# Kernel optimization log

Hardware: AMD Instinct MI355X
Metric: run time of the kernel (lower is better)

The kernel has to match this reference:

```python
import jax, jax.numpy as jnp
import numpy as np

N_NEIGHBORS = 3


def square_distance(src, dst):
    # src: [B,N,3], dst: [B,M,3] -> [B,N,M]
    d = -2.0 * jnp.einsum('bnc,bmc->bnm', src, dst)
    d = d + jnp.sum(src * src, axis=-1)[:, :, None]
    d = d + jnp.sum(dst * dst, axis=-1)[:, None, :]
    return d


def setup_inputs() -> dict:
    key = jax.random.key(0)
    k1, k2, k3 = jax.random.split(key, 3)
    B, N_q, N_k, C = 4, 8192, 2048, 128
    xyz_q = jax.random.normal(k1, (B, N_q, 3), dtype=jnp.float32)
    xyz_k = jax.random.normal(k2, (B, N_k, 3), dtype=jnp.float32)
    v_k = jax.random.normal(k3, (B, N_k, C), dtype=jnp.float32)
    return {"xyz_q": xyz_q, "xyz_k": xyz_k, "v_k": v_k}


def reference(xyz_q, xyz_k, v_k):
    # pairwise squared distances [B,N_q,N_k]
    sqrdists = square_distance(xyz_q, xyz_k)
    # kNN: smallest nsample distances per query
    neg_dist, idx = jax.lax.top_k(-sqrdists, N_NEIGHBORS)  # [B,N_q,k]
    dist_nearest = jnp.take_along_axis(sqrdists, idx, axis=2)
    dist_nearest = jnp.maximum(dist_nearest, 1e-10)
    weights = 1.0 / dist_nearest
    weights = weights / jnp.sum(weights, axis=-1, keepdims=True)
    # gather neighbor features: [B,N_q,k,C]
    grouped_v = jax.vmap(lambda v, i: v[i])(v_k, idx)
    # inverse-distance-weighted interpolation
    v_q = jnp.einsum('bnk,bnkc->bnc', weights, grouped_v)
    return v_q
```

## Files before the change

kernel.cpp:

```cpp
#include <hip/hip_runtime.h>
#include <cfloat>

#define BB 4
#define NQ 8192
#define NK 2048
#define CC 128
#define C4 (CC / 4)

#define QPB 64
#define SPLITS 16
#define KPS (NK / SPLITS)
#define KPAD 2
#define KROW (KPS + KPAD)
#define QPT 4
#define NTHR (QPB * SPLITS / QPT)
#define RD_ROW 68

typedef float v2f __attribute__((ext_vector_type(2)));

static __device__ __forceinline__ float fmed3(float a, float b, float c) {
    return __builtin_amdgcn_fmed3f(a, b, c);
}

__global__ __launch_bounds__(256) void pack_keys(
    const float* __restrict__ xyz_k, float4* __restrict__ keys)
{
    int i = blockIdx.x * 256 + threadIdx.x;
    if (i < BB * NK) {
        float x = xyz_k[i * 3 + 0];
        float y = xyz_k[i * 3 + 1];
        float z = xyz_k[i * 3 + 2];
        keys[i] = make_float4(x, y, z, fmaf(x, x, fmaf(y, y, z * z)));
    }
}

__global__ __launch_bounds__(NTHR, 2) void fp_main(
    const float*  __restrict__ xyz_q,
    const float4* __restrict__ keys,
    const float4* __restrict__ vk,
    float4*       __restrict__ out)
{
    __shared__ float4  ks[SPLITS * KROW];
    __shared__ unsigned rd[QPB][RD_ROW];
    __shared__ float   sw[QPB][4];
    __shared__ int     si[QPB][4];

    const int b     = blockIdx.y;
    const int qbase = blockIdx.x * QPB;
    const int tid   = threadIdx.x;
    const int split = tid >> 4;
    const int g     = tid & 15;

    #pragma unroll
    for (int i = tid; i < NK; i += NTHR)
        ks[(i >> 7) * KROW + (i & (KPS - 1))] = keys[(size_t)b * NK + i];

    v2f AX[2], AY[2], AZ[2], QB[2];
    #pragma unroll
    for (int qi = 0; qi < QPT; ++qi) {
        int q = qbase + g + 16 * qi;
        float qx = xyz_q[(b * NQ + q) * 3 + 0];
        float qy = xyz_q[(b * NQ + q) * 3 + 1];
        float qz = xyz_q[(b * NQ + q) * 3 + 2];
        AX[qi >> 1][qi & 1] = -2.0f * qx;
        AY[qi >> 1][qi & 1] = -2.0f * qy;
        AZ[qi >> 1][qi & 1] = -2.0f * qz;
        QB[qi >> 1][qi & 1] = fmaf(qx, qx, fmaf(qy, qy, qz * qz)) + 1.0e-3f;
    }
    __syncthreads();

    const int kbase = split * KROW;
    const int kbeg  = split * KPS;

    float u[QPT][4];
    #pragma unroll
    for (int qi = 0; qi < QPT; ++qi)
        u[qi][0] = u[qi][1] = u[qi][2] = u[qi][3] = FLT_MAX;

    #pragma unroll 8
    for (int j = 0; j < KPS; ++j) {
        float4 kk = ks[kbase + j];
        unsigned kidx = (unsigned)(kbeg + j);
        v2f kx2 = { kk.x, kk.x }, ky2 = { kk.y, kk.y };
        v2f kz2 = { kk.z, kk.z }, kw2 = { kk.w, kk.w };
        #pragma unroll
        for (int pr = 0; pr < 2; ++pr) {
            v2f t2 = __builtin_elementwise_fma(AX[pr], kx2,
                     __builtin_elementwise_fma(AY[pr], ky2,
                     __builtin_elementwise_fma(AZ[pr], kz2, QB[pr]))) + kw2;
            #pragma unroll
            for (int h = 0; h < 2; ++h) {
                int qi = pr * 2 + h;
                float p = __uint_as_float(
                    (__float_as_uint(t2[h]) & 0xFFFFF800u) | kidx);
                u[qi][3] = fmed3(p, u[qi][2], u[qi][3]);
                u[qi][2] = fmed3(p, u[qi][1], u[qi][2]);
                u[qi][1] = fmed3(p, u[qi][0], u[qi][1]);
                u[qi][0] = fminf(u[qi][0], p);
            }
        }
    }

    #pragma unroll
    for (int qi = 0; qi < QPT; ++qi) {
        int ql = g + 16 * qi;
        uint4 v = make_uint4(__float_as_uint(u[qi][0]), __float_as_uint(u[qi][1]),
                             __float_as_uint(u[qi][2]), __float_as_uint(u[qi][3]));
        *(uint4*)&rd[ql][split * 4] = v;
    }
    __syncthreads();

    if (tid < QPB) {
        const int ql = tid;
        float m[8];
        #pragma unroll
        for (int c = 0; c < 8; ++c) m[c] = FLT_MAX;
        #pragma unroll 4
        for (int i = 0; i < SPLITS; ++i) {
            uint4 v = *(const uint4*)&rd[ql][i * 4];
            unsigned vv[4] = { v.x, v.y, v.z, v.w };
            #pragma unroll
            for (int c = 0; c < 4; ++c) {
                float p = __uint_as_float(vv[c]);
                m[7] = fmed3(p, m[6], m[7]);
                m[6] = fmed3(p, m[5], m[6]);
                m[5] = fmed3(p, m[4], m[5]);
                m[4] = fmed3(p, m[3], m[4]);
                m[3] = fmed3(p, m[2], m[3]);
                m[2] = fmed3(p, m[1], m[2]);
                m[1] = fmed3(p, m[0], m[1]);
                m[0] = fminf(m[0], p);
            }
        }
        int q = qbase + ql;
        double qx = (double)xyz_q[(b * NQ + q) * 3 + 0];
        double qy = (double)xyz_q[(b * NQ + q) * 3 + 1];
        double qz = (double)xyz_q[(b * NQ + q) * 3 + 2];
        double M0 = DBL_MAX, M1 = DBL_MAX, M2 = DBL_MAX;
        #pragma unroll
        for (int c = 0; c < 8; ++c) {
            unsigned ki = __float_as_uint(m[c]) & 0x7FFu;
            float4 ka = ks[(ki >> 7) * KROW + (ki & (KPS - 1))];
            double dx = qx - (double)ka.x;
            double dy = qy - (double)ka.y;
            double dz = qz - (double)ka.z;
            double dd = dx * dx + dy * dy + dz * dz;
            double x = __longlong_as_double(
                (long long)((((unsigned long long)__double_as_longlong(dd)) & ~0x7FFull)
                            | (unsigned long long)ki));
            double a1 = fmax(x, M1), a0 = fmax(x, M0);
            M2 = fmin(M2, a1);
            M1 = fmin(M1, a0);
            M0 = fmin(M0, x);
        }
        unsigned long long b0 = (unsigned long long)__double_as_longlong(M0);
        unsigned long long b1 = (unsigned long long)__double_as_longlong(M1);
        unsigned long long b2 = (unsigned long long)__double_as_longlong(M2);
        double e0 = __longlong_as_double((long long)(b0 & ~0x7FFull));
        double e1 = __longlong_as_double((long long)(b1 & ~0x7FFull));
        double e2 = __longlong_as_double((long long)(b2 & ~0x7FFull));
        e0 = fmax(e0, 1e-10);
        e1 = fmax(e1, 1e-10);
        e2 = fmax(e2, 1e-10);
        double w0 = 1.0 / e0, w1 = 1.0 / e1, w2 = 1.0 / e2;
        double s  = w0 + w1 + w2;
        sw[ql][0] = (float)(w0 / s);
        sw[ql][1] = (float)(w1 / s);
        sw[ql][2] = (float)(w2 / s);
        si[ql][0] = (int)(b0 & 0x7FFull);
        si[ql][1] = (int)(b1 & 0x7FFull);
        si[ql][2] = (int)(b2 & 0x7FFull);
    }
    __syncthreads();

    const float4* vb = vk + (size_t)b * NK * C4;
    float4* ob = out + ((size_t)b * NQ + qbase) * C4;
    #pragma unroll
    for (int r = 0; r < (QPB * C4) / NTHR; ++r) {
        int o  = r * NTHR + tid;
        int qq = o >> 5;
        int c4 = o & (C4 - 1);
        float w0 = sw[qq][0], w1 = sw[qq][1], w2 = sw[qq][2];
        int   j0 = si[qq][0], j1 = si[qq][1], j2 = si[qq][2];
        float4 v0 = vb[j0 * C4 + c4];
        float4 v1 = vb[j1 * C4 + c4];
        float4 v2 = vb[j2 * C4 + c4];
        float4 res;
        res.x = fmaf(w0, v0.x, fmaf(w1, v1.x, w2 * v2.x));
        res.y = fmaf(w0, v0.y, fmaf(w1, v1.y, w2 * v2.y));
        res.z = fmaf(w0, v0.z, fmaf(w1, v1.z, w2 * v2.z));
        res.w = fmaf(w0, v0.w, fmaf(w1, v1.w, w2 * v2.w));
        ob[o] = res;
    }
}

extern "C" void kernel_launch(void* const* d_in, const int* in_sizes, int n_in,
                              void* d_out, int out_size, void* d_ws, size_t ws_size,
                              hipStream_t stream)
{
    const float* xyz_q = (const float*)d_in[0];
    const float* xyz_k = (const float*)d_in[1];
    const float* v_k   = (const float*)d_in[2];

    float4* keys = (float4*)d_ws;

    pack_keys<<<dim3((BB * NK + 255) / 256), dim3(256), 0, stream>>>(xyz_k, keys);
    fp_main<<<dim3(NQ / QPB, BB), dim3(NTHR), 0, stream>>>(
        xyz_q, keys, (const float4*)v_k, (float4*)d_out);
}
```

Measured before the change: 93.12 us.

## Fuse key packing into kNN kernel and split gather into separate kernel

Drops the pack_keys pre-pass: each kNN block now reads the raw xyz_k array and computes the squared norms itself while filling shared memory. The weighted gather is moved out of the kNN kernel into its own fully parallel kernel, with weights and indices passed through workspace. The aim is to stop the gather tail of each block from serializing behind the compute-bound kNN phase, and to let the gather run with full occupancy. The cost is an extra workspace write and read, a second launch, and redundant per-block key packing.

```diff
diff --git a/kernel.cpp b/kernel.cpp
--- a/kernel.cpp
+++ b/kernel.cpp
@@ -22,28 +22,14 @@
     return __builtin_amdgcn_fmed3f(a, b, c);
 }
 
-__global__ __launch_bounds__(256) void pack_keys(
-    const float* __restrict__ xyz_k, float4* __restrict__ keys)
-{
-    int i = blockIdx.x * 256 + threadIdx.x;
-    if (i < BB * NK) {
-        float x = xyz_k[i * 3 + 0];
-        float y = xyz_k[i * 3 + 1];
-        float z = xyz_k[i * 3 + 2];
-        keys[i] = make_float4(x, y, z, fmaf(x, x, fmaf(y, y, z * z)));
-    }
-}
-
-__global__ __launch_bounds__(NTHR, 2) void fp_main(
+__global__ __launch_bounds__(NTHR, 2) void fp_knn(
     const float*  __restrict__ xyz_q,
-    const float4* __restrict__ keys,
-    const float4* __restrict__ vk,
-    float4*       __restrict__ out)
+    const float*  __restrict__ xyz_k,
+    float4*       __restrict__ wsw,
+    int4*         __restrict__ wsi)
 {
     __shared__ float4  ks[SPLITS * KROW];
     __shared__ unsigned rd[QPB][RD_ROW];
-    __shared__ float   sw[QPB][4];
-    __shared__ int     si[QPB][4];
 
     const int b     = blockIdx.y;
     const int qbase = blockIdx.x * QPB;
@@ -51,9 +37,17 @@
     const int split = tid >> 4;
     const int g     = tid & 15;
 
-    #pragma unroll
-    for (int i = tid; i < NK; i += NTHR)
-        ks[(i >> 7) * KROW + (i & (KPS - 1))] = keys[(size_t)b * NK + i];
+    {
+        const float* kb = xyz_k + (size_t)b * NK * 3;
+        #pragma unroll
+        for (int i = tid; i < NK; i += NTHR) {
+            float x = kb[i * 3 + 0];
+            float y = kb[i * 3 + 1];
+            float z = kb[i * 3 + 2];
+            ks[(i >> 7) * KROW + (i & (KPS - 1))] =
+                make_float4(x, y, z, fmaf(x, x, fmaf(y, y, z * z)));
+        }
+    }
 
     v2f AX[2], AY[2], AZ[2], QB[2];
     #pragma unroll
@@ -164,34 +158,36 @@
         e2 = fmax(e2, 1e-10);
         double w0 = 1.0 / e0, w1 = 1.0 / e1, w2 = 1.0 / e2;
         double s  = w0 + w1 + w2;
-        sw[ql][0] = (float)(w0 / s);
-        sw[ql][1] = (float)(w1 / s);
-        sw[ql][2] = (float)(w2 / s);
-        si[ql][0] = (int)(b0 & 0x7FFull);
-        si[ql][1] = (int)(b1 & 0x7FFull);
-        si[ql][2] = (int)(b2 & 0x7FFull);
-    }
-    __syncthreads();
-
+        int qg = b * NQ + q;
+        wsw[qg] = make_float4((float)(w0 / s), (float)(w1 / s), (float)(w2 / s), 0.0f);
+        wsi[qg] = make_int4((int)(b0 & 0x7FFull), (int)(b1 & 0x7FFull),
+                            (int)(b2 & 0x7FFull), 0);
+    }
+}
+
+__global__ __launch_bounds__(256) void fp_gather(
+    const float4* __restrict__ vk,
+    const float4* __restrict__ wsw,
+    const int4*   __restrict__ wsi,
+    float4*       __restrict__ out)
+{
+    int o  = blockIdx.x * 256 + threadIdx.x;
+    int q  = o >> 5;
+    int c4 = o & (C4 - 1);
+    int b  = q >> 13;
+
+    float4 w = wsw[q];
+    int4   j = wsi[q];
     const float4* vb = vk + (size_t)b * NK * C4;
-    float4* ob = out + ((size_t)b * NQ + qbase) * C4;
-    #pragma unroll
-    for (int r = 0; r < (QPB * C4) / NTHR; ++r) {
-        int o  = r * NTHR + tid;
-        int qq = o >> 5;
-        int c4 = o & (C4 - 1);
-        float w0 = sw[qq][0], w1 = sw[qq][1], w2 = sw[qq][2];
-        int   j0 = si[qq][0], j1 = si[qq][1], j2 = si[qq][2];
-        float4 v0 = vb[j0 * C4 + c4];
-        float4 v1 = vb[j1 * C4 + c4];
-        float4 v2 = vb[j2 * C4 + c4];
-        float4 res;
-        res.x = fmaf(w0, v0.x, fmaf(w1, v1.x, w2 * v2.x));
-        res.y = fmaf(w0, v0.y, fmaf(w1, v1.y, w2 * v2.y));
-        res.z = fmaf(w0, v0.z, fmaf(w1, v1.z, w2 * v2.z));
-        res.w = fmaf(w0, v0.w, fmaf(w1, v1.w, w2 * v2.w));
-        ob[o] = res;
-    }
+    float4 v0 = vb[j.x * C4 + c4];
+    float4 v1 = vb[j.y * C4 + c4];
+    float4 v2 = vb[j.z * C4 + c4];
+    float4 res;
+    res.x = fmaf(w.x, v0.x, fmaf(w.y, v1.x, w.z * v2.x));
+    res.y = fmaf(w.x, v0.y, fmaf(w.y, v1.y, w.z * v2.y));
+    res.z = fmaf(w.x, v0.z, fmaf(w.y, v1.z, w.z * v2.z));
+    res.w = fmaf(w.x, v0.w, fmaf(w.y, v1.w, w.z * v2.w));
+    out[o] = res;
 }
 
 extern "C" void kernel_launch(void* const* d_in, const int* in_sizes, int n_in,
@@ -202,9 +198,11 @@
     const float* xyz_k = (const float*)d_in[1];
     const float* v_k   = (const float*)d_in[2];
 
-    float4* keys = (float4*)d_ws;
-
-    pack_keys<<<dim3((BB * NK + 255) / 256), dim3(256), 0, stream>>>(xyz_k, keys);
-    fp_main<<<dim3(NQ / QPB, BB), dim3(NTHR), 0, stream>>>(
-        xyz_q, keys, (const float4*)v_k, (float4*)d_out);
-}
+    char* ws = (char*)d_ws;
+    float4* wsw = (float4*)ws;
+    int4*   wsi = (int4*)(ws + (1u << 20));
+
+    fp_knn<<<dim3(NQ / QPB, BB), dim3(NTHR), 0, stream>>>(xyz_q, xyz_k, wsw, wsi);
+    fp_gather<<<dim3(BB * NQ * C4 / 256), dim3(256), 0, stream>>>(
+        (const float4*)v_k, wsw, wsi, (float4*)d_out);
+}
```

Result: no change. 94.42 us (+1.4%).
